# Performance work log

Hardware: AMD Instinct MI355X
Metric: run time of the kernel (lower is better)

Reference implementation:

```python
import jax, jax.numpy as jnp
import numpy as np

N = 100000   # nodes
E = 1600000  # edges
D = 128      # hidden_dim (also input feature dim)
R = 8        # num_relations
B = 4        # num_bases
OUT = 64     # out_dim
P = 2        # gating exponent p


def setup_inputs() -> dict:
    key = jax.random.key(0)
    ks = jax.random.split(key, 16)
    w = lambda k, shape, s=0.05: jax.random.normal(k, shape, dtype=jnp.float32) * s
    return {
        "x": jax.random.normal(ks[0], (N, D), dtype=jnp.float32),
        "src": jax.random.randint(ks[1], (E,), 0, N, dtype=jnp.int32),
        "dst": jax.random.randint(ks[2], (E,), 0, N, dtype=jnp.int32),
        "edge_type": jax.random.randint(ks[3], (E,), 0, R, dtype=jnp.int32),
        "proj_W": w(ks[4], (D, D)), "proj_b": jnp.zeros((D,), jnp.float32),
        "basis1": w(ks[5], (B, D, D)), "comp1": w(ks[6], (R, B), 1.0),
        "root1": w(ks[7], (D, D)), "bias1": jnp.zeros((D,), jnp.float32),
        "basis2": w(ks[8], (B, D, D)), "comp2": w(ks[9], (R, B), 1.0),
        "root2": w(ks[10], (D, D)), "bias2": jnp.zeros((D,), jnp.float32),
        "out_W": w(ks[11], (D, OUT)), "out_b": jnp.zeros((OUT,), jnp.float32),
    }


def _rgcn(x, src, dst, et, basis, comp, root, bias):
    # PyG RGCNConv (basis decomposition, aggr='mean'):
    # out_i = x_i @ root + bias + sum_r mean_{e: dst=i, type=r}( x_{src_e} @ W_r )
    # Mean is linear, so aggregate raw features per (node, relation), then matmul.
    n, d = x.shape
    seg = dst * R + et                                   # combined (node, relation) key
    agg = jax.ops.segment_sum(x[src], seg, num_segments=n * R).reshape(n, R, d)
    cnt = jax.ops.segment_sum(jnp.ones(seg.shape, x.dtype), seg, num_segments=n * R).reshape(n, R)
    agg = agg / jnp.maximum(cnt, 1.0)[:, :, None]        # empty segments -> 0
    W = jnp.einsum('rb,bdf->rdf', comp, basis)           # [R, D, D] relation weights
    return jnp.einsum('nrd,rdf->nf', agg, W) + x @ root + bias


def _gate(x, src, dst):
    # tau = tanh(scatter_mean(|x_src - x_dst|^p, index=src))
    diff = jnp.abs(x[src] - x[dst]) ** P                 # [E, D]
    s = jax.ops.segment_sum(diff, src, num_segments=x.shape[0])
    c = jax.ops.segment_sum(jnp.ones(src.shape, x.dtype), src, num_segments=x.shape[0])
    return jnp.tanh(s / jnp.maximum(c, 1.0)[:, None])


def reference(x, src, dst, edge_type, proj_W, proj_b,
              basis1, comp1, root1, bias1,
              basis2, comp2, root2, bias2,
              out_W, out_b):
    # input projection (dropout is identity in eval mode)
    h = jax.nn.relu(x @ proj_W + proj_b)
    latents = [h]
    for basis, comp, root, bias in ((basis1, comp1, root1, bias1),
                                    (basis2, comp2, root2, bias2)):
        h_new = jax.nn.relu(_rgcn(h, src, dst, edge_type, basis, comp, root, bias))
        tau = _gate(h, src, dst)
        h = (1.0 - tau) * h + tau * h_new
        latents.append(h)
    out = h @ out_W + out_b
    return (out, jnp.stack(latents))
```

## Files before the change

### kernel.cpp

```cpp
#include <hip/hip_runtime.h>
#include <cstdint>
#include <cstddef>

#define D 128
#define RR 8

typedef __attribute__((ext_vector_type(8))) short short8;
typedef __attribute__((ext_vector_type(4))) float f32x4;

__device__ inline ushort f2b(float x) {
    union { float f; unsigned u; } v; v.f = x;
    unsigned r = v.u + 0x7fff + ((v.u >> 16) & 1);
    return (ushort)(r >> 16);
}
__device__ inline float b2f(ushort u) {
    union { unsigned u; float f; } v; v.u = ((unsigned)u) << 16; return v.f;
}

__device__ inline void gload_lds16(const ushort* g, ushort* l) {
    __builtin_amdgcn_global_load_lds(
        (const __attribute__((address_space(1))) unsigned int*)g,
        (__attribute__((address_space(3))) unsigned int*)l, 16, 0, 0);
}

template<bool BIAS, bool RELU, bool STF, bool STB>
__global__ __launch_bounds__(256, 4) void gemm_bf16(
    const ushort* __restrict__ A0, int lda0, int k0steps,
    const ushort* __restrict__ A1, int lda1,
    const ushort* __restrict__ BT, int ktiles,
    const float* __restrict__ bias, float* __restrict__ Cf, int ldcf,
    ushort* __restrict__ Cb, int ldcb, int M, int ncol)
{
    __shared__ ushort As[128 * 64];
    __shared__ ushort Bs[128 * 64];
    const int tid = threadIdx.x;
    const int m0 = blockIdx.x * 128;
    const int ldb = ktiles * 128;
    const int ksteps = ktiles * 2;

    const int w = tid >> 6, lane = tid & 63;
    const int wm = (w & 1) * 64, wn = (w >> 1) * 64;
    const int l15 = lane & 15, quad = lane >> 4;

    const ushort* a0p[4];
    const ushort* a1p[4];
    const ushort* bp[4];
#pragma unroll
    for (int it = 0; it < 4; it++) {
        int gi = w * 256 + it * 64 + lane;
        int row = gi >> 3, g = gi & 7;
        int cg = g ^ (row & 7);
        int gr = m0 + row; if (gr > M - 1) gr = M - 1;
        a0p[it] = A0 + (size_t)gr * lda0 + (cg << 3);
        a1p[it] = A1 + (size_t)gr * lda1 + (cg << 3);
        bp[it]  = BT + (size_t)row * ldb + (cg << 3);
    }

    f32x4 acc[4][4];
    const f32x4 z4 = {0.f, 0.f, 0.f, 0.f};
#pragma unroll
    for (int i = 0; i < 4; i++)
#pragma unroll
        for (int j = 0; j < 4; j++) acc[i][j] = z4;

    for (int kt = 0; kt < ksteps; kt++) {
        const int ko = kt * 64;
        if (kt < k0steps) {
#pragma unroll
            for (int it = 0; it < 4; it++)
                gload_lds16(a0p[it] + ko, As + w * 2048 + it * 512);
        } else {
            const int ko1 = (kt - k0steps) * 64;
#pragma unroll
            for (int it = 0; it < 4; it++)
                gload_lds16(a1p[it] + ko1, As + w * 2048 + it * 512);
        }
#pragma unroll
        for (int it = 0; it < 4; it++)
            gload_lds16(bp[it] + ko, Bs + w * 2048 + it * 512);
        __syncthreads();

#pragma unroll
        for (int ks = 0; ks < 64; ks += 32) {
            const int q0 = (ks >> 3) + quad;
            short8 af[4], bfr[4];
#pragma unroll
            for (int i = 0; i < 4; i++) {
                int row = wm + i * 16 + l15;
                af[i] = *(const short8*)(&As[row * 64 + ((q0 ^ (row & 7)) << 3)]);
            }
#pragma unroll
            for (int j = 0; j < 4; j++) {
                int row = wn + j * 16 + l15;
                bfr[j] = *(const short8*)(&Bs[row * 64 + ((q0 ^ (row & 7)) << 3)]);
            }
#pragma unroll
            for (int i = 0; i < 4; i++)
#pragma unroll
                for (int j = 0; j < 4; j++)
                    acc[i][j] = __builtin_amdgcn_mfma_f32_16x16x32_bf16(
                        af[i], bfr[j], acc[i][j], 0, 0, 0);
        }
        __syncthreads();
    }

#pragma unroll
    for (int i = 0; i < 4; i++) {
#pragma unroll
        for (int q = 0; q < 4; q++) {
            int gm = m0 + wm + i * 16 + quad * 4 + q;
            if (gm >= M) continue;
#pragma unroll
            for (int j = 0; j < 4; j++) {
                int gn = wn + j * 16 + l15;
                if (gn >= ncol) continue;
                float v = acc[i][j][q];
                if (BIAS) v += bias[gn];
                if (RELU) v = v > 0.f ? v : 0.f;
                if (STF) Cf[(size_t)gm * ldcf + gn] = v;
                if (STB) Cb[(size_t)gm * ldcb + gn] = f2b(v);
            }
        }
    }
}

__global__ void build_bigBT(const float* __restrict__ basis,
                            const float* __restrict__ comp,
                            const float* __restrict__ root,
                            ushort* __restrict__ BT)
{
    int i = blockIdx.x * 256 + threadIdx.x;
    if (i >= 128 * 1152) return;
    int f = i / 1152, c = i - f * 1152;
    float a;
    if (c < 1024) {
        int r = c >> 7, d = c & 127;
        a = 0.f;
#pragma unroll
        for (int b = 0; b < 4; b++)
            a += comp[r * 4 + b] * basis[(b * 128 + d) * 128 + f];
    } else {
        a = root[(c - 1024) * 128 + f];
    }
    BT[i] = f2b(a);
}

__global__ void transpose_pad(const float* __restrict__ in, ushort* __restrict__ out,
                              int cols)
{
    int i = blockIdx.x * 256 + threadIdx.x;
    if (i >= 128 * 128) return;
    int k = i & 127, f = i >> 7;
    out[i] = (f < cols) ? f2b(in[k * cols + f]) : (ushort)0;
}

__global__ void cast_x(const float* __restrict__ in, ushort* __restrict__ Hc, int total4)
{
    int i = blockIdx.x * 256 + threadIdx.x;
    if (i >= total4) return;
    float4 v = ((const float4*)in)[i];
    ushort4 o = { f2b(v.x), f2b(v.y), f2b(v.z), f2b(v.w) };
    *(ushort4*)(Hc + (size_t)i * 4) = o;
}

__global__ void count_slot(const int* __restrict__ src, const int* __restrict__ dst,
                           const int* __restrict__ et, int* __restrict__ cnt,
                           int* __restrict__ deg, int* __restrict__ slotA,
                           int* __restrict__ slotG, int E)
{
    int t = blockIdx.x * 256 + threadIdx.x;
    int e0 = t * 4;
    if (e0 + 4 <= E) {
        int4 s4 = ((const int4*)src)[t];
        int4 d4 = ((const int4*)dst)[t];
        int4 t4 = ((const int4*)et)[t];
        int4 sa, sg;
        sa.x = atomicAdd(&cnt[d4.x * RR + t4.x], 1);
        sa.y = atomicAdd(&cnt[d4.y * RR + t4.y], 1);
        sa.z = atomicAdd(&cnt[d4.z * RR + t4.z], 1);
        sa.w = atomicAdd(&cnt[d4.w * RR + t4.w], 1);
        sg.x = atomicAdd(&deg[s4.x], 1);
        sg.y = atomicAdd(&deg[s4.y], 1);
        sg.z = atomicAdd(&deg[s4.z], 1);
        sg.w = atomicAdd(&deg[s4.w], 1);
        ((int4*)slotA)[t] = sa;
        ((int4*)slotG)[t] = sg;
    } else {
        for (int e = e0; e < E; e++) {
            slotA[e] = atomicAdd(&cnt[dst[e] * RR + et[e]], 1);
            slotG[e] = atomicAdd(&deg[src[e]], 1);
        }
    }
}

__global__ void scan1(const int* __restrict__ in, int* __restrict__ bsum, int n)
{
    __shared__ int s[256];
    const int b = blockIdx.x, t = threadIdx.x;
    const int base = b * 1024;
    int v = 0;
#pragma unroll
    for (int i = 0; i < 4; i++) {
        int idx = base + t * 4 + i;
        if (idx < n) v += in[idx];
    }
    s[t] = v; __syncthreads();
    for (int off = 128; off > 0; off >>= 1) {
        if (t < off) s[t] += s[t + off];
        __syncthreads();
    }
    if (t == 0) bsum[b] = s[0];
}

__global__ void scan_top(int* __restrict__ bsum, int nb)
{
    __shared__ int s[1024];
    const int t = threadIdx.x;
    int v = (t < nb) ? bsum[t] : 0;
    s[t] = v; __syncthreads();
    for (int off = 1; off < 1024; off <<= 1) {
        int x = (t >= off) ? s[t - off] : 0;
        __syncthreads();
        s[t] += x;
        __syncthreads();
    }
    if (t < nb) bsum[t] = s[t] - v;
}

__global__ void scan2(const int* __restrict__ in, const int* __restrict__ bsum,
                      int* __restrict__ out, int n)
{
    __shared__ int s[256];
    const int b = blockIdx.x, t = threadIdx.x;
    const int base = b * 1024;
    int loc[4];
    int v = 0;
#pragma unroll
    for (int i = 0; i < 4; i++) {
        int idx = base + t * 4 + i;
        int x = (idx < n) ? in[idx] : 0;
        loc[i] = v; v += x;
    }
    s[t] = v; __syncthreads();
    for (int off = 1; off < 256; off <<= 1) {
        int x = (t >= off) ? s[t - off] : 0;
        __syncthreads();
        s[t] += x;
        __syncthreads();
    }
    const int add = bsum[b] + (s[t] - v);
#pragma unroll
    for (int i = 0; i < 4; i++) {
        int idx = base + t * 4 + i;
        if (idx < n) out[idx] = add + loc[i];
    }
}

__global__ void fill_scatter(const int* __restrict__ src, const int* __restrict__ dst,
                             const int* __restrict__ et,
                             const int* __restrict__ aoff, const int* __restrict__ goff,
                             const int* __restrict__ slotA, const int* __restrict__ slotG,
                             int* __restrict__ acsr, int* __restrict__ gcsr, int E)
{
    int t = blockIdx.x * 256 + threadIdx.x;
    int e0 = t * 4;
    if (e0 + 4 <= E) {
        int4 s4 = ((const int4*)src)[t];
        int4 d4 = ((const int4*)dst)[t];
        int4 t4 = ((const int4*)et)[t];
        int4 sa = ((const int4*)slotA)[t];
        int4 sg = ((const int4*)slotG)[t];
        acsr[aoff[d4.x * RR + t4.x] + sa.x] = s4.x;
        acsr[aoff[d4.y * RR + t4.y] + sa.y] = s4.y;
        acsr[aoff[d4.z * RR + t4.z] + sa.z] = s4.z;
        acsr[aoff[d4.w * RR + t4.w] + sa.w] = s4.w;
        gcsr[goff[s4.x] + sg.x] = d4.x;
        gcsr[goff[s4.y] + sg.y] = d4.y;
        gcsr[goff[s4.z] + sg.z] = d4.z;
        gcsr[goff[s4.w] + sg.w] = d4.w;
    } else {
        for (int e = e0; e < E; e++) {
            int s0 = src[e], d0 = dst[e];
            acsr[aoff[d0 * RR + et[e]] + slotA[e]] = s0;
            gcsr[goff[s0] + slotG[e]] = d0;
        }
    }
}

__global__ __launch_bounds__(256) void gate_gather(
    const ushort* __restrict__ Hc, const int* __restrict__ gcsr,
    const int* __restrict__ goff, const int* __restrict__ deg,
    ushort* __restrict__ TAUb, int N)
{
    const int g = threadIdx.x >> 4, lane = threadIdx.x & 15;
    const int n = blockIdx.x * 16 + g;
    if (n >= N) return;
    const int start = goff[n];
    const int c = deg[n];
    const ushort* hbase = Hc + lane * 8;
    const short8 a8 = *(const short8*)(hbase + (size_t)n * 128);
    float av[8];
#pragma unroll
    for (int j = 0; j < 8; j++) av[j] = b2f((ushort)a8[j]);
    float acc[8];
#pragma unroll
    for (int j = 0; j < 8; j++) acc[j] = 0.f;

    int i = 0;
    for (; i + 4 <= c; i += 4) {
        int d0 = gcsr[start + i],     d1 = gcsr[start + i + 1];
        int d2 = gcsr[start + i + 2], d3 = gcsr[start + i + 3];
        short8 b0 = *(const short8*)(hbase + (size_t)d0 * 128);
        short8 b1 = *(const short8*)(hbase + (size_t)d1 * 128);
        short8 b2 = *(const short8*)(hbase + (size_t)d2 * 128);
        short8 b3 = *(const short8*)(hbase + (size_t)d3 * 128);
#pragma unroll
        for (int j = 0; j < 8; j++) {
            float dx0 = av[j] - b2f((ushort)b0[j]);
            float dx1 = av[j] - b2f((ushort)b1[j]);
            float dx2 = av[j] - b2f((ushort)b2[j]);
            float dx3 = av[j] - b2f((ushort)b3[j]);
            acc[j] += dx0 * dx0 + dx1 * dx1 + dx2 * dx2 + dx3 * dx3;
        }
    }
    if (i + 2 <= c) {
        int d0 = gcsr[start + i], d1 = gcsr[start + i + 1];
        short8 b0 = *(const short8*)(hbase + (size_t)d0 * 128);
        short8 b1 = *(const short8*)(hbase + (size_t)d1 * 128);
#pragma unroll
        for (int j = 0; j < 8; j++) {
            float dx0 = av[j] - b2f((ushort)b0[j]);
            float dx1 = av[j] - b2f((ushort)b1[j]);
            acc[j] += dx0 * dx0 + dx1 * dx1;
        }
        i += 2;
    }
    if (i < c) {
        int d0 = gcsr[start + i];
        short8 b0 = *(const short8*)(hbase + (size_t)d0 * 128);
#pragma unroll
        for (int j = 0; j < 8; j++) {
            float dx0 = av[j] - b2f((ushort)b0[j]);
            acc[j] += dx0 * dx0;
        }
    }
    const float inv = (c > 0) ? (1.f / (float)c) : 1.f;
    short8 t;
#pragma unroll
    for (int j = 0; j < 8; j++) t[j] = (short)f2b(tanhf(acc[j] * inv));
    *(short8*)(TAUb + (size_t)n * D + lane * 8) = t;
}

__global__ __launch_bounds__(256) void agg_gather(
    ushort* __restrict__ Agg, const ushort* __restrict__ Hc,
    const int* __restrict__ acsr, const int* __restrict__ aoff,
    const int* __restrict__ cnt, int N)
{
    const int g = threadIdx.x >> 4, lane = threadIdx.x & 15;
    const int n = blockIdx.x * 16 + g;
    if (n >= N) return;
    const int sbase = n * RR;
    const int start = aoff[sbase];
    int ctot = 0;
#pragma unroll
    for (int r0 = 0; r0 < RR; r0++) ctot += cnt[sbase + r0];

    const ushort* hbase = Hc + lane * 8;
    ushort* obase = Agg + (size_t)n * 1024 + lane * 8;

    float cum[8];
#pragma unroll
    for (int j = 0; j < 8; j++) cum[j] = 0.f;
    int r = 0;
    int segstart = 0;
    int nexte = cnt[sbase];

    auto flush = [&]() {
        int c = nexte - segstart;
        short8 outv = {0, 0, 0, 0, 0, 0, 0, 0};
        if (c > 0) {
            float inv = 1.f / (float)c;
#pragma unroll
            for (int j = 0; j < 8; j++) outv[j] = (short)f2b(cum[j] * inv);
        }
        __builtin_nontemporal_store(outv, (short8*)(obase + r * 128));
#pragma unroll
        for (int j = 0; j < 8; j++) cum[j] = 0.f;
        segstart = nexte;
        r++;
        if (r < RR) nexte += cnt[sbase + r];
    };

    int i = 0;
    for (; i + 4 <= ctot; i += 4) {
        int s0 = acsr[start + i],     s1 = acsr[start + i + 1];
        int s2 = acsr[start + i + 2], s3 = acsr[start + i + 3];
        short8 y0 = *(const short8*)(hbase + (size_t)s0 * 128);
        short8 y1 = *(const short8*)(hbase + (size_t)s1 * 128);
        short8 y2 = *(const short8*)(hbase + (size_t)s2 * 128);
        short8 y3 = *(const short8*)(hbase + (size_t)s3 * 128);
        while (i >= nexte) flush();
#pragma unroll
        for (int j = 0; j < 8; j++) cum[j] += b2f((ushort)y0[j]);
        while (i + 1 >= nexte) flush();
#pragma unroll
        for (int j = 0; j < 8; j++) cum[j] += b2f((ushort)y1[j]);
        while (i + 2 >= nexte) flush();
#pragma unroll
        for (int j = 0; j < 8; j++) cum[j] += b2f((ushort)y2[j]);
        while (i + 3 >= nexte) flush();
#pragma unroll
        for (int j = 0; j < 8; j++) cum[j] += b2f((ushort)y3[j]);
    }
    for (; i < ctot; i++) {
        int s0 = acsr[start + i];
        short8 y0 = *(const short8*)(hbase + (size_t)s0 * 128);
        while (i >= nexte) flush();
#pragma unroll
        for (int j = 0; j < 8; j++) cum[j] += b2f((ushort)y0[j]);
    }
    while (r < RR) flush();
}

__global__ void finalize(const float* __restrict__ hp, float* __restrict__ hn,
                         const ushort* __restrict__ TAUb, ushort* __restrict__ Hc,
                         int total4)
{
    int idx = blockIdx.x * 256 + threadIdx.x;
    if (idx >= total4) return;
    const float4 p = ((const float4*)hp)[idx];
    const float4 a = ((const float4*)hn)[idx];
    const ushort4 t4 = ((const ushort4*)TAUb)[idx];
    float4 o;
    o.x = p.x + b2f(t4.x) * (a.x - p.x);
    o.y = p.y + b2f(t4.y) * (a.y - p.y);
    o.z = p.z + b2f(t4.z) * (a.z - p.z);
    o.w = p.w + b2f(t4.w) * (a.w - p.w);
    ((float4*)hn)[idx] = o;
    ushort4 ob = { f2b(o.x), f2b(o.y), f2b(o.z), f2b(o.w) };
    *(ushort4*)(Hc + (size_t)idx * 4) = ob;
}

extern "C" void kernel_launch(void* const* d_in, const int* in_sizes, int n_in,
                              void* d_out, int out_size, void* d_ws, size_t ws_size,
                              hipStream_t stream)
{
    const float* x      = (const float*)d_in[0];
    const int*   src    = (const int*)  d_in[1];
    const int*   dst    = (const int*)  d_in[2];
    const int*   etyp   = (const int*)  d_in[3];
    const float* projW  = (const float*)d_in[4];
    const float* projb  = (const float*)d_in[5];
    const float* basis1 = (const float*)d_in[6];
    const float* comp1  = (const float*)d_in[7];
    const float* root1  = (const float*)d_in[8];
    const float* bias1  = (const float*)d_in[9];
    const float* basis2 = (const float*)d_in[10];
    const float* comp2  = (const float*)d_in[11];
    const float* root2  = (const float*)d_in[12];
    const float* bias2  = (const float*)d_in[13];
    const float* outW   = (const float*)d_in[14];
    const float* outb   = (const float*)d_in[15];

    const int N    = in_sizes[0] / D;
    const int E    = in_sizes[1];
    const int OUTD = in_sizes[15];

    float* out  = (float*)d_out;
    float* lat0 = out + (size_t)N * OUTD;
    float* lat1 = lat0 + (size_t)N * D;
    float* lat2 = lat1 + (size_t)N * D;

    char* p = (char*)d_ws;
    ushort* Agg   = (ushort*)p;  p += (size_t)N * 1024 * 2;
    ushort* Hc    = (ushort*)p;  p += (size_t)N * 128 * 2;
    ushort* TAUb  = (ushort*)p;  p += (size_t)N * D * 2;
    ushort* projWT = (ushort*)p; p += 16384 * 2;
    ushort* outWT  = (ushort*)p; p += 16384 * 2;
    ushort* bigBT1 = (ushort*)p; p += (size_t)128 * 1152 * 2;
    ushort* bigBT2 = (ushort*)p; p += (size_t)128 * 1152 * 2;
    int* cnt_i  = (int*)p;       p += (size_t)N * RR * 4;
    int* deg_i  = (int*)p;       p += (size_t)N * 4;
    int* aoff   = (int*)p;       p += (size_t)N * RR * 4;
    int* goff   = (int*)p;       p += (size_t)N * 4;
    int* slotA  = (int*)p;       p += (size_t)E * 4;
    int* slotG  = (int*)p;       p += (size_t)E * 4;
    int* acsr   = (int*)p;       p += (size_t)E * 4;
    int* gcsr   = (int*)p;       p += (size_t)E * 4;
    int* bsum   = (int*)p;       p += 4096;

    if ((size_t)(p - (char*)d_ws) > ws_size) return;

    hipMemsetAsync(cnt_i, 0, sizeof(int) * ((size_t)N * RR + N), stream);

    build_bigBT<<<(128 * 1152 + 255) / 256, 256, 0, stream>>>(basis1, comp1, root1, bigBT1);
    build_bigBT<<<(128 * 1152 + 255) / 256, 256, 0, stream>>>(basis2, comp2, root2, bigBT2);
    transpose_pad<<<64, 256, 0, stream>>>(projW, projWT, 128);
    transpose_pad<<<64, 256, 0, stream>>>(outW, outWT, OUTD);

    cast_x<<<(N * 32 + 255) / 256, 256, 0, stream>>>(x, Hc, N * 32);

    count_slot<<<(E / 4 + 255) / 256, 256, 0, stream>>>(
        src, dst, etyp, cnt_i, deg_i, slotA, slotG, E);

    {
        int n1 = N * RR, nb1 = (n1 + 1023) / 1024;
        scan1<<<nb1, 256, 0, stream>>>(cnt_i, bsum, n1);
        scan_top<<<1, 1024, 0, stream>>>(bsum, nb1);
        scan2<<<nb1, 256, 0, stream>>>(cnt_i, bsum, aoff, n1);
        int nb2 = (N + 1023) / 1024;
        scan1<<<nb2, 256, 0, stream>>>(deg_i, bsum, N);
        scan_top<<<1, 1024, 0, stream>>>(bsum, nb2);
        scan2<<<nb2, 256, 0, stream>>>(deg_i, bsum, goff, N);
    }

    fill_scatter<<<(E / 4 + 255) / 256, 256, 0, stream>>>(
        src, dst, etyp, aoff, goff, slotA, slotG, acsr, gcsr, E);

    const int mb = (N + 127) / 128;
    const int nodeblocks16 = (N + 15) / 16;

    gemm_bf16<true, true, true, true><<<mb, 256, 0, stream>>>(
        Hc, 128, 2, Hc, 128, projWT, 1, projb, lat0, 128, Hc, 128, N, 128);

    const ushort* bigBT[2] = {bigBT1, bigBT2};
    const float* biases[2] = {bias1, bias2};
    float* lats[3]         = {lat0, lat1, lat2};

    for (int l = 0; l < 2; l++) {
        float* hn = lats[l + 1];

        gate_gather<<<nodeblocks16, 256, 0, stream>>>(Hc, gcsr, goff, deg_i, TAUb, N);
        agg_gather<<<nodeblocks16, 256, 0, stream>>>(Agg, Hc, acsr, aoff, cnt_i, N);

        gemm_bf16<true, true, true, false><<<mb, 256, 0, stream>>>(
            Agg, 1024, 16, Hc, 128, bigBT[l], 9, biases[l], hn, 128, nullptr, 0, N, 128);

        finalize<<<(N * 32 + 255) / 256, 256, 0, stream>>>(
            lats[l], hn, TAUb, Hc, N * 32);
    }

    gemm_bf16<true, false, true, false><<<mb, 256, 0, stream>>>(
        Hc, 128, 2, Hc, 128, outWT, 1, outb, out, OUTD, nullptr, 0, N, OUTD);
}
```

Before: 1.020 ms.

## Fuse gating blend into GEMM epilogue and merge gate/agg gathers into one launch

The separate finalize kernel is removed. The tau-weighted blend with the previous latent, and the bf16 copy written back to Hc, now happen in the layer GEMM epilogue through a new GATE template flag. This avoids a full extra read and write pass over the fp32 hidden states in each layer. The gate and aggregation gather kernels are also merged into one launch that splits work by block index, so both gathers can run at the same time. The epilogue now reads hp and TAU with strided scalar loads and overwrites Hc rows that the same block read as A1 earlier; this is safe only because each block touches only its own row tile.

```diff
diff --git a/kernel.cpp b/kernel.cpp
--- a/kernel.cpp
+++ b/kernel.cpp
@@ -23,13 +23,15 @@
         (__attribute__((address_space(3))) unsigned int*)l, 16, 0, 0);
 }
 
-template<bool BIAS, bool RELU, bool STF, bool STB>
+template<bool BIAS, bool RELU, bool STF, bool STB, bool GATE>
 __global__ __launch_bounds__(256, 4) void gemm_bf16(
     const ushort* __restrict__ A0, int lda0, int k0steps,
     const ushort* __restrict__ A1, int lda1,
     const ushort* __restrict__ BT, int ktiles,
     const float* __restrict__ bias, float* __restrict__ Cf, int ldcf,
-    ushort* __restrict__ Cb, int ldcb, int M, int ncol)
+    ushort* __restrict__ Cb, int ldcb,
+    const float* __restrict__ hp, const ushort* __restrict__ TAU,
+    int M, int ncol)
 {
     __shared__ ushort As[128 * 64];
     __shared__ ushort Bs[128 * 64];
@@ -117,6 +119,11 @@
                 float v = acc[i][j][q];
                 if (BIAS) v += bias[gn];
                 if (RELU) v = v > 0.f ? v : 0.f;
+                if (GATE) {
+                    float pv  = hp[(size_t)gm * 128 + gn];
+                    float tau = b2f(TAU[(size_t)gm * 128 + gn]);
+                    v = pv + tau * (v - pv);
+                }
                 if (STF) Cf[(size_t)gm * ldcf + gn] = v;
                 if (STB) Cb[(size_t)gm * ldcb + gn] = f2b(v);
             }
@@ -287,158 +294,137 @@
     }
 }
 
-__global__ __launch_bounds__(256) void gate_gather(
-    const ushort* __restrict__ Hc, const int* __restrict__ gcsr,
-    const int* __restrict__ goff, const int* __restrict__ deg,
-    ushort* __restrict__ TAUb, int N)
-{
-    const int g = threadIdx.x >> 4, lane = threadIdx.x & 15;
-    const int n = blockIdx.x * 16 + g;
-    if (n >= N) return;
-    const int start = goff[n];
-    const int c = deg[n];
-    const ushort* hbase = Hc + lane * 8;
-    const short8 a8 = *(const short8*)(hbase + (size_t)n * 128);
-    float av[8];
-#pragma unroll
-    for (int j = 0; j < 8; j++) av[j] = b2f((ushort)a8[j]);
-    float acc[8];
-#pragma unroll
-    for (int j = 0; j < 8; j++) acc[j] = 0.f;
-
-    int i = 0;
-    for (; i + 4 <= c; i += 4) {
-        int d0 = gcsr[start + i],     d1 = gcsr[start + i + 1];
-        int d2 = gcsr[start + i + 2], d3 = gcsr[start + i + 3];
-        short8 b0 = *(const short8*)(hbase + (size_t)d0 * 128);
-        short8 b1 = *(const short8*)(hbase + (size_t)d1 * 128);
-        short8 b2 = *(const short8*)(hbase + (size_t)d2 * 128);
-        short8 b3 = *(const short8*)(hbase + (size_t)d3 * 128);
-#pragma unroll
-        for (int j = 0; j < 8; j++) {
-            float dx0 = av[j] - b2f((ushort)b0[j]);
-            float dx1 = av[j] - b2f((ushort)b1[j]);
-            float dx2 = av[j] - b2f((ushort)b2[j]);
-            float dx3 = av[j] - b2f((ushort)b3[j]);
-            acc[j] += dx0 * dx0 + dx1 * dx1 + dx2 * dx2 + dx3 * dx3;
-        }
-    }
-    if (i + 2 <= c) {
-        int d0 = gcsr[start + i], d1 = gcsr[start + i + 1];
-        short8 b0 = *(const short8*)(hbase + (size_t)d0 * 128);
-        short8 b1 = *(const short8*)(hbase + (size_t)d1 * 128);
-#pragma unroll
-        for (int j = 0; j < 8; j++) {
-            float dx0 = av[j] - b2f((ushort)b0[j]);
-            float dx1 = av[j] - b2f((ushort)b1[j]);
-            acc[j] += dx0 * dx0 + dx1 * dx1;
-        }
-        i += 2;
-    }
-    if (i < c) {
-        int d0 = gcsr[start + i];
-        short8 b0 = *(const short8*)(hbase + (size_t)d0 * 128);
-#pragma unroll
-        for (int j = 0; j < 8; j++) {
-            float dx0 = av[j] - b2f((ushort)b0[j]);
-            acc[j] += dx0 * dx0;
-        }
-    }
-    const float inv = (c > 0) ? (1.f / (float)c) : 1.f;
-    short8 t;
-#pragma unroll
-    for (int j = 0; j < 8; j++) t[j] = (short)f2b(tanhf(acc[j] * inv));
-    *(short8*)(TAUb + (size_t)n * D + lane * 8) = t;
-}
-
-__global__ __launch_bounds__(256) void agg_gather(
+__global__ __launch_bounds__(256) void gathers(
     ushort* __restrict__ Agg, const ushort* __restrict__ Hc,
     const int* __restrict__ acsr, const int* __restrict__ aoff,
-    const int* __restrict__ cnt, int N)
+    const int* __restrict__ cnt,
+    const int* __restrict__ gcsr, const int* __restrict__ goff,
+    const int* __restrict__ deg, ushort* __restrict__ TAUb,
+    int N, int nbA)
 {
     const int g = threadIdx.x >> 4, lane = threadIdx.x & 15;
-    const int n = blockIdx.x * 16 + g;
-    if (n >= N) return;
-    const int sbase = n * RR;
-    const int start = aoff[sbase];
-    int ctot = 0;
-#pragma unroll
-    for (int r0 = 0; r0 < RR; r0++) ctot += cnt[sbase + r0];
-
-    const ushort* hbase = Hc + lane * 8;
-    ushort* obase = Agg + (size_t)n * 1024 + lane * 8;
-
-    float cum[8];
-#pragma unroll
-    for (int j = 0; j < 8; j++) cum[j] = 0.f;
-    int r = 0;
-    int segstart = 0;
-    int nexte = cnt[sbase];
-
-    auto flush = [&]() {
-        int c = nexte - segstart;
-        short8 outv = {0, 0, 0, 0, 0, 0, 0, 0};
-        if (c > 0) {
-            float inv = 1.f / (float)c;
-#pragma unroll
-            for (int j = 0; j < 8; j++) outv[j] = (short)f2b(cum[j] * inv);
-        }
-        __builtin_nontemporal_store(outv, (short8*)(obase + r * 128));
+    if (blockIdx.x < nbA) {
+        const int n = blockIdx.x * 16 + g;
+        if (n >= N) return;
+        const int sbase = n * RR;
+        const int start = aoff[sbase];
+        int ctot = 0;
+#pragma unroll
+        for (int r0 = 0; r0 < RR; r0++) ctot += cnt[sbase + r0];
+
+        const ushort* hbase = Hc + lane * 8;
+        ushort* obase = Agg + (size_t)n * 1024 + lane * 8;
+
+        float cum[8];
 #pragma unroll
         for (int j = 0; j < 8; j++) cum[j] = 0.f;
-        segstart = nexte;
-        r++;
-        if (r < RR) nexte += cnt[sbase + r];
-    };
-
-    int i = 0;
-    for (; i + 4 <= ctot; i += 4) {
-        int s0 = acsr[start + i],     s1 = acsr[start + i + 1];
-        int s2 = acsr[start + i + 2], s3 = acsr[start + i + 3];
-        short8 y0 = *(const short8*)(hbase + (size_t)s0 * 128);
-        short8 y1 = *(const short8*)(hbase + (size_t)s1 * 128);
-        short8 y2 = *(const short8*)(hbase + (size_t)s2 * 128);
-        short8 y3 = *(const short8*)(hbase + (size_t)s3 * 128);
-        while (i >= nexte) flush();
-#pragma unroll
-        for (int j = 0; j < 8; j++) cum[j] += b2f((ushort)y0[j]);
-        while (i + 1 >= nexte) flush();
-#pragma unroll
-        for (int j = 0; j < 8; j++) cum[j] += b2f((ushort)y1[j]);
-        while (i + 2 >= nexte) flush();
-#pragma unroll
-        for (int j = 0; j < 8; j++) cum[j] += b2f((ushort)y2[j]);
-        while (i + 3 >= nexte) flush();
-#pragma unroll
-        for (int j = 0; j < 8; j++) cum[j] += b2f((ushort)y3[j]);
-    }
-    for (; i < ctot; i++) {
-        int s0 = acsr[start + i];
-        short8 y0 = *(const short8*)(hbase + (size_t)s0 * 128);
-        while (i >= nexte) flush();
-#pragma unroll
-        for (int j = 0; j < 8; j++) cum[j] += b2f((ushort)y0[j]);
-    }
-    while (r < RR) flush();
-}
-
-__global__ void finalize(const float* __restrict__ hp, float* __restrict__ hn,
-                         const ushort* __restrict__ TAUb, ushort* __restrict__ Hc,
-                         int total4)
-{
-    int idx = blockIdx.x * 256 + threadIdx.x;
-    if (idx >= total4) return;
-    const float4 p = ((const float4*)hp)[idx];
-    const float4 a = ((const float4*)hn)[idx];
-    const ushort4 t4 = ((const ushort4*)TAUb)[idx];
-    float4 o;
-    o.x = p.x + b2f(t4.x) * (a.x - p.x);
-    o.y = p.y + b2f(t4.y) * (a.y - p.y);
-    o.z = p.z + b2f(t4.z) * (a.z - p.z);
-    o.w = p.w + b2f(t4.w) * (a.w - p.w);
-    ((float4*)hn)[idx] = o;
-    ushort4 ob = { f2b(o.x), f2b(o.y), f2b(o.z), f2b(o.w) };
-    *(ushort4*)(Hc + (size_t)idx * 4) = ob;
+        int r = 0;
+        int segstart = 0;
+        int nexte = cnt[sbase];
+
+        auto flush = [&]() {
+            int c = nexte - segstart;
+            short8 outv = {0, 0, 0, 0, 0, 0, 0, 0};
+            if (c > 0) {
+                float inv = 1.f / (float)c;
+#pragma unroll
+                for (int j = 0; j < 8; j++) outv[j] = (short)f2b(cum[j] * inv);
+            }
+            __builtin_nontemporal_store(outv, (short8*)(obase + r * 128));
+#pragma unroll
+            for (int j = 0; j < 8; j++) cum[j] = 0.f;
+            segstart = nexte;
+            r++;
+            if (r < RR) nexte += cnt[sbase + r];
+        };
+
+        int i = 0;
+        for (; i + 4 <= ctot; i += 4) {
+            int s0 = acsr[start + i],     s1 = acsr[start + i + 1];
+            int s2 = acsr[start + i + 2], s3 = acsr[start + i + 3];
+            short8 y0 = *(const short8*)(hbase + (size_t)s0 * 128);
+            short8 y1 = *(const short8*)(hbase + (size_t)s1 * 128);
+            short8 y2 = *(const short8*)(hbase + (size_t)s2 * 128);
+            short8 y3 = *(const short8*)(hbase + (size_t)s3 * 128);
+            while (i >= nexte) flush();
+#pragma unroll
+            for (int j = 0; j < 8; j++) cum[j] += b2f((ushort)y0[j]);
+            while (i + 1 >= nexte) flush();
+#pragma unroll
+            for (int j = 0; j < 8; j++) cum[j] += b2f((ushort)y1[j]);
+            while (i + 2 >= nexte) flush();
+#pragma unroll
+            for (int j = 0; j < 8; j++) cum[j] += b2f((ushort)y2[j]);
+            while (i + 3 >= nexte) flush();
+#pragma unroll
+            for (int j = 0; j < 8; j++) cum[j] += b2f((ushort)y3[j]);
+        }
+        for (; i < ctot; i++) {
+            int s0 = acsr[start + i];
+            short8 y0 = *(const short8*)(hbase + (size_t)s0 * 128);
+            while (i >= nexte) flush();
+#pragma unroll
+            for (int j = 0; j < 8; j++) cum[j] += b2f((ushort)y0[j]);
+        }
+        while (r < RR) flush();
+    } else {
+        const int n = (blockIdx.x - nbA) * 16 + g;
+        if (n >= N) return;
+        const int start = goff[n];
+        const int c = deg[n];
+        const ushort* hbase = Hc + lane * 8;
+        const short8 a8 = *(const short8*)(hbase + (size_t)n * 128);
+        float av[8];
+#pragma unroll
+        for (int j = 0; j < 8; j++) av[j] = b2f((ushort)a8[j]);
+        float acc[8];
+#pragma unroll
+        for (int j = 0; j < 8; j++) acc[j] = 0.f;
+
+        int i = 0;
+        for (; i + 4 <= c; i += 4) {
+            int d0 = gcsr[start + i],     d1 = gcsr[start + i + 1];
+            int d2 = gcsr[start + i + 2], d3 = gcsr[start + i + 3];
+            short8 b0 = *(const short8*)(hbase + (size_t)d0 * 128);
+            short8 b1 = *(const short8*)(hbase + (size_t)d1 * 128);
+            short8 b2 = *(const short8*)(hbase + (size_t)d2 * 128);
+            short8 b3 = *(const short8*)(hbase + (size_t)d3 * 128);
+#pragma unroll
+            for (int j = 0; j < 8; j++) {
+                float dx0 = av[j] - b2f((ushort)b0[j]);
+                float dx1 = av[j] - b2f((ushort)b1[j]);
+                float dx2 = av[j] - b2f((ushort)b2[j]);
+                float dx3 = av[j] - b2f((ushort)b3[j]);
+                acc[j] += dx0 * dx0 + dx1 * dx1 + dx2 * dx2 + dx3 * dx3;
+            }
+        }
+        if (i + 2 <= c) {
+            int d0 = gcsr[start + i], d1 = gcsr[start + i + 1];
+            short8 b0 = *(const short8*)(hbase + (size_t)d0 * 128);
+            short8 b1 = *(const short8*)(hbase + (size_t)d1 * 128);
+#pragma unroll
+            for (int j = 0; j < 8; j++) {
+                float dx0 = av[j] - b2f((ushort)b0[j]);
+                float dx1 = av[j] - b2f((ushort)b1[j]);
+                acc[j] += dx0 * dx0 + dx1 * dx1;
+            }
+            i += 2;
+        }
+        if (i < c) {
+            int d0 = gcsr[start + i];
+            short8 b0 = *(const short8*)(hbase + (size_t)d0 * 128);
+#pragma unroll
+            for (int j = 0; j < 8; j++) {
+                float dx0 = av[j] - b2f((ushort)b0[j]);
+                acc[j] += dx0 * dx0;
+            }
+        }
+        const float inv = (c > 0) ? (1.f / (float)c) : 1.f;
+        short8 t;
+#pragma unroll
+        for (int j = 0; j < 8; j++) t[j] = (short)f2b(tanhf(acc[j] * inv));
+        *(short8*)(TAUb + (size_t)n * D + lane * 8) = t;
+    }
 }
 
 extern "C" void kernel_launch(void* const* d_in, const int* in_sizes, int n_in,
@@ -518,10 +504,11 @@
         src, dst, etyp, aoff, goff, slotA, slotG, acsr, gcsr, E);
 
     const int mb = (N + 127) / 128;
-    const int nodeblocks16 = (N + 15) / 16;
-
-    gemm_bf16<true, true, true, true><<<mb, 256, 0, stream>>>(
-        Hc, 128, 2, Hc, 128, projWT, 1, projb, lat0, 128, Hc, 128, N, 128);
+    const int nbA = (N + 15) / 16;
+
+    gemm_bf16<true, true, true, true, false><<<mb, 256, 0, stream>>>(
+        Hc, 128, 2, Hc, 128, projWT, 1, projb, lat0, 128, Hc, 128,
+        nullptr, nullptr, N, 128);
 
     const ushort* bigBT[2] = {bigBT1, bigBT2};
     const float* biases[2] = {bias1, bias2};
@@ -530,16 +517,15 @@
     for (int l = 0; l < 2; l++) {
         float* hn = lats[l + 1];
 
-        gate_gather<<<nodeblocks16, 256, 0, stream>>>(Hc, gcsr, goff, deg_i, TAUb, N);
-        agg_gather<<<nodeblocks16, 256, 0, stream>>>(Agg, Hc, acsr, aoff, cnt_i, N);
-
-        gemm_bf16<true, true, true, false><<<mb, 256, 0, stream>>>(
-            Agg, 1024, 16, Hc, 128, bigBT[l], 9, biases[l], hn, 128, nullptr, 0, N, 128);
-
-        finalize<<<(N * 32 + 255) / 256, 256, 0, stream>>>(
-            lats[l], hn, TAUb, Hc, N * 32);
-    }
-
-    gemm_bf16<true, false, true, false><<<mb, 256, 0, stream>>>(
-        Hc, 128, 2, Hc, 128, outWT, 1, outb, out, OUTD, nullptr, 0, N, OUTD);
-}
+        gathers<<<2 * nbA, 256, 0, stream>>>(
+            Agg, Hc, acsr, aoff, cnt_i, gcsr, goff, deg_i, TAUb, N, nbA);
+
+        gemm_bf16<true, true, true, true, true><<<mb, 256, 0, stream>>>(
+            Agg, 1024, 16, Hc, 128, bigBT[l], 9, biases[l], hn, 128, Hc, 128,
+            lats[l], TAUb, N, 128);
+    }
+
+    gemm_bf16<true, false, true, false, false><<<mb, 256, 0, stream>>>(
+        Hc, 128, 2, Hc, 128, outWT, 1, outb, out, OUTD, nullptr, 0,
+        nullptr, nullptr, N, OUTD);
+}
```

Result: faster. 998.2 us (-2.2%).
